# Optimization experiments

Measured on AMD Instinct MI355X. Metric: run time of the kernel, lower is better.

## Reference

```python
import jax, jax.numpy as jnp
import numpy as np

N, E, G, B, L = 24576, 98304, 512, 512, 1000
F_IN, H1, C1, C2, HID = 5, 2, 64, 128, 256


def setup_inputs() -> dict:
    key = jax.random.key(0)
    ks = jax.random.split(key, 20)
    rn = lambda k, s: jax.random.normal(k, s, jnp.float32) * 0.1
    return {
        "x": jax.random.normal(ks[0], (N, F_IN), jnp.float32),
        "edge_index": jax.random.randint(ks[1], (2, E), 0, N),
        "batch": jnp.sort(jax.random.randint(ks[2], (N,), 0, G)),
        "protein_seq": jax.random.randint(ks[3], (B, L), 0, 22),
        "W1": rn(ks[4], (F_IN, H1 * C1)), "att_src1": rn(ks[5], (H1, C1)), "att_dst1": rn(ks[6], (H1, C1)), "b1": jnp.zeros((H1 * C1,), jnp.float32),
        "W2": rn(ks[7], (H1 * C1, C2)), "att_src2": rn(ks[8], (1, C2)), "att_dst2": rn(ks[9], (1, C2)), "b2": jnp.zeros((C2,), jnp.float32),
        "Wd": rn(ks[10], (C2, HID)), "bd": jnp.zeros((HID,), jnp.float32),
        "Pe": rn(ks[11], (22, 64)),
        "K1": rn(ks[12], (64, 64, 3)), "bk1": jnp.zeros((64,), jnp.float32),
        "K2": rn(ks[13], (128, 64, 5)), "bk2": jnp.zeros((128,), jnp.float32),
        "Wp": rn(ks[14], (128, HID)), "bp": jnp.zeros((HID,), jnp.float32),
        "Wf1": rn(ks[15], (2 * HID, 128)), "bf1": jnp.zeros((128,), jnp.float32),
        "Wf2": rn(ks[16], (128, 64)), "bf2": jnp.zeros((64,), jnp.float32),
        "Wo": rn(ks[17], (64, 1)), "bo": jnp.zeros((1,), jnp.float32),
    }


def _gat(x, edge_index, W, att_src, att_dst, b, heads, out_ch):
    """PyG GATConv: add self-loops, per-edge LeakyReLU(0.2) scores, segment softmax over dst."""
    n = x.shape[0]
    h = (x @ W).reshape(n, heads, out_ch)
    loop = jnp.arange(n)
    src = jnp.concatenate([edge_index[0], loop])
    dst = jnp.concatenate([edge_index[1], loop])
    a_s = jnp.sum(h * att_src[None], axis=-1)  # [n, H]
    a_d = jnp.sum(h * att_dst[None], axis=-1)
    e = jax.nn.leaky_relu(a_s[src] + a_d[dst], negative_slope=0.2)  # [E+n, H]
    m = jax.ops.segment_max(e, dst, num_segments=n)
    w = jnp.exp(e - m[dst])
    den = jax.ops.segment_sum(w, dst, num_segments=n)
    alpha = w / (den[dst] + 1e-16)
    out = jax.ops.segment_sum(h[src] * alpha[..., None], dst, num_segments=n)
    return out.reshape(n, heads * out_ch) + b


def _conv1d(x, k, pad):  # x: [B,C,L], k: [O,I,K]
    return jax.lax.conv_general_dilated(x, k, (1,), [(pad, pad)], dimension_numbers=("NCH", "OIH", "NCH"))


def reference(x, edge_index, batch, protein_seq, W1, att_src1, att_dst1, b1, W2, att_src2, att_dst2, b2, Wd, bd, Pe, K1, bk1, K2, bk2, Wp, bp, Wf1, bf1, Wf2, bf2, Wo, bo):
    # drug branch (GAT x2 + global mean pool)
    g = jax.nn.elu(_gat(x, edge_index, W1, att_src1, att_dst1, b1, H1, C1))
    g = jax.nn.elu(_gat(g, edge_index, W2, att_src2, att_dst2, b2, 1, C2))
    sums = jax.ops.segment_sum(g, batch, num_segments=G)
    cnt = jax.ops.segment_sum(jnp.ones((g.shape[0], 1), g.dtype), batch, num_segments=G)
    drug = jax.nn.relu(sums / jnp.maximum(cnt, 1.0) @ Wd + bd)
    # protein branch (embed -> conv1d x2 -> global max pool)
    pe = Pe[protein_seq].transpose(0, 2, 1)  # [B, 64, L]
    p = jax.nn.elu(_conv1d(pe, K1, 1) + bk1[None, :, None])
    p = jax.nn.elu(_conv1d(p, K2, 2) + bk2[None, :, None])
    prot = jax.nn.relu(jnp.max(p, axis=2) @ Wp + bp)
    # head
    h = jnp.concatenate([drug, prot], axis=1)
    h = jax.nn.relu(h @ Wf1 + bf1)
    h = jax.nn.relu(h @ Wf2 + bf2)
    return h @ Wo + bo
```

## Files before the change

### kernel.cpp

```cpp
#include <hip/hip_runtime.h>
#include <hip/hip_bf16.h>
#include <math.h>

#define NN 24576
#define NE 98304
#define ETOT (NE + NN)
#define NG 512
#define NB 512
#define LL 1000
#define TL 124
#define NTILE 9
#define PROT_BLKS (NB * NTILE)
#define CNT_BLKS (ETOT / 256)
#define AS1_BLKS (NN * 2 / 256)

typedef __attribute__((ext_vector_type(8))) short short8;
typedef __attribute__((ext_vector_type(4))) short short4v;
typedef __attribute__((ext_vector_type(4))) float f32x4;

__device__ inline short f2bf(float x) {
    union { __hip_bfloat16 b; short s; } u;
    u.b = __float2bfloat16(x);
    return u.s;
}

__device__ inline float bf2f(short s) {
    return __uint_as_float(((unsigned)(unsigned short)s) << 16);
}

__device__ inline void atomicMaxFloat(float* addr, float val) {
    int* ai = (int*)addr;
    int old = __float_as_int(*addr);
    while (__int_as_float(old) < val) {
        int assumed = old;
        old = atomicCAS(ai, assumed, __float_as_int(val));
        if (old == assumed) break;
    }
}

__global__ void k_init_prep(int* deg, int* cursor, float* sums, float* cnt, float* pmax,
                            const float* K1, const float* K2, const float* W2, const float* Pe,
                            const float* W1, const float* as1c, const float* ad1c,
                            const float* as2c, const float* ad2c,
                            short* Bswz1, short* Bswz2, short* Bh2, short* Bl2, short* Peb,
                            float* wvec) {
    int bid = blockIdx.x, t = threadIdx.x;
    if (bid < 256) {
        int i = bid * 256 + t;
        if (i < NN) { deg[i] = 0; cursor[i] = 0; }
        if (i < NG * 128) sums[i] = 0.f;
        if (i < NG) cnt[i] = 0.f;
        if (i < NB * 128) pmax[i] = -1e30f;
        return;
    }
    int idx = (bid - 256) * 256 + t;
    if (idx < 22 * 64) Peb[idx] = f2bf(Pe[idx]);
    if (idx < 20) {
        int q = idx % 10, hd = q / 5, f = q % 5;
        const float* av = (idx < 10) ? as1c : ad1c;
        float s = 0.f;
        for (int c = 0; c < 64; c++) s += W1[f * 128 + hd * 64 + c] * av[hd * 64 + c];
        wvec[idx < 10 ? q : 10 + q] = s;
    }
    if (idx >= 32 && idx < 288) {
        int q = idx - 32;
        int kk = q & 127;
        const float* av = (q < 128) ? as2c : ad2c;
        float s = 0.f;
        for (int n2 = 0; n2 < 128; n2++) s += W2[kk * 128 + n2] * av[n2];
        wvec[idx] = s;
    }
    if (idx < 192 * 64) {
        int j = idx & 7, lane = (idx >> 3) & 63, rest = idx >> 9;
        int nt = rest & 3, kb = rest >> 2;
        int k = kb * 32 + ((lane >> 4) << 3) + j;
        int n = nt * 16 + (lane & 15);
        int kk = k >> 6, i = k & 63;
        Bswz1[idx] = f2bf(K1[n * 192 + i * 3 + kk]);
    }
    if (idx < 320 * 128) {
        int j = idx & 7, lane = (idx >> 3) & 63, rest = idx >> 9;
        int nt = rest & 7, kb = rest >> 3;
        int k = kb * 32 + ((lane >> 4) << 3) + j;
        int n = nt * 16 + (lane & 15);
        int kk = k / 64, i = k % 64;
        Bswz2[idx] = f2bf(K2[n * 320 + i * 5 + kk]);
    }
    if (idx < 128 * 128) {
        int j = idx & 7, lane = (idx >> 3) & 63, rest = idx >> 9;
        int nt = rest & 7, kb = rest >> 3;
        int k = kb * 32 + ((lane >> 4) << 3) + j;
        int n = nt * 16 + (lane & 15);
        float v = W2[k * 128 + n];
        short hh = f2bf(v);
        Bh2[idx] = hh;
        Bl2[idx] = f2bf(v - bf2f(hh));
    }
}

#define SSTR 72
__global__ __launch_bounds__(256, 4) void k_prot_cnt_as1(
    const int* seq, const short* Peb, const short* Bswz1, const float* bk1,
    const short* Bswz2, const float* bk2, float* pmax,
    const int* ei, int* deg,
    const float* x, const float* wvec, float* as1o, float* ad1o) {
    int bid = blockIdx.x;
    int t = threadIdx.x;

    if (bid >= PROT_BLKS) {
        int rb = bid - PROT_BLKS;
        if (rb < CNT_BLKS) {
            int e = rb * 256 + t;
            int d = (e < NE) ? ei[NE + e] : e - NE;
            atomicAdd(&deg[d], 1);
        } else {
            int idx = (rb - CNT_BLKS) * 256 + t;
            int n = idx >> 1, hd = idx & 1;
            float s = 0.f, dv = 0.f;
#pragma unroll
            for (int f = 0; f < 5; f++) {
                float xv = x[n * 5 + f];
                s += xv * wvec[hd * 5 + f];
                dv += xv * wvec[10 + hd * 5 + f];
            }
            as1o[idx] = s;
            ad1o[idx] = dv;
        }
        return;
    }

    __shared__ __align__(16) short sEmb[130 * SSTR];
    __shared__ __align__(16) short s1[132 * SSTR];

    int b = bid / NTILE;
    int tile = bid - b * NTILE;
    int t0 = tile * TL;
    int wv = t >> 6, lane = t & 63;
    int ln15 = lane & 15, quad = lane >> 4;
    int mhalf = wv & 1, nhalf = wv >> 1;

    for (int j0 = 0; j0 < 130; j0 += 64) {
        int j = j0 + (t >> 2);
        if (j < 130) {
            int c0 = (t & 3) * 16;
            int l = t0 - 3 + j;
            int id = (l >= 0 && l < LL) ? seq[b * LL + l] : -1;
            short* dst = &sEmb[j * SSTR + c0];
            if (id >= 0) {
                const short8* src = (const short8*)&Peb[id * 64 + c0];
                *(short8*)dst = src[0];
                *(short8*)(dst + 8) = src[1];
            } else {
                *(short8*)dst = (short8){0, 0, 0, 0, 0, 0, 0, 0};
                *(short8*)(dst + 8) = (short8){0, 0, 0, 0, 0, 0, 0, 0};
            }
        }
    }
    s1[(128 + (t >> 6)) * SSTR + (t & 63)] = 0;
    __syncthreads();

    {
        f32x4 acc[4][2];
#pragma unroll
        for (int mi = 0; mi < 4; mi++)
#pragma unroll
            for (int ni = 0; ni < 2; ni++) acc[mi][ni] = (f32x4){0.f, 0.f, 0.f, 0.f};
#pragma unroll
        for (int kb = 0; kb < 6; kb++) {
            int koff = kb * 32 + quad * 8;
            int kk = koff >> 6, i0 = koff & 63;
            short8 b0 = *(const short8*)&Bswz1[((kb * 4 + nhalf * 2 + 0) * 64 + lane) * 8];
            short8 b1 = *(const short8*)&Bswz1[((kb * 4 + nhalf * 2 + 1) * 64 + lane) * 8];
#pragma unroll
            for (int mi = 0; mi < 4; mi++) {
                int arow = (mhalf * 4 + mi) * 16 + ln15 + kk;
                short8 a = *(const short8*)&sEmb[arow * SSTR + i0];
                acc[mi][0] = __builtin_amdgcn_mfma_f32_16x16x32_bf16(a, b0, acc[mi][0], 0, 0, 0);
                acc[mi][1] = __builtin_amdgcn_mfma_f32_16x16x32_bf16(a, b1, acc[mi][1], 0, 0, 0);
            }
        }
#pragma unroll
        for (int mi = 0; mi < 4; mi++) {
            int mt = mhalf * 4 + mi;
#pragma unroll
            for (int ni = 0; ni < 2; ni++) {
                int col = (nhalf * 2 + ni) * 16 + ln15;
                float bias = bk1[col];
#pragma unroll
                for (int r = 0; r < 4; r++) {
                    int q = mt * 16 + quad * 4 + r;
                    int l = t0 - 2 + q;
                    float v = acc[mi][ni][r] + bias;
                    v = v > 0.f ? v : __expf(v) - 1.f;
                    s1[q * SSTR + col] = (l >= 0 && l < LL) ? f2bf(v) : (short)0;
                }
            }
        }
    }
    __syncthreads();

    f32x4 acc2[4][4];
#pragma unroll
    for (int mi = 0; mi < 4; mi++)
#pragma unroll
        for (int ni = 0; ni < 4; ni++) acc2[mi][ni] = (f32x4){0.f, 0.f, 0.f, 0.f};
#pragma unroll 2
    for (int kb = 0; kb < 10; kb++) {
        int koff = kb * 32 + quad * 8;
        int kk = koff >> 6, i0 = koff & 63;
        short8 a[4], bb[4];
#pragma unroll
        for (int mi = 0; mi < 4; mi++) {
            int arow = (mhalf * 4 + mi) * 16 + ln15 + kk;
            a[mi] = *(const short8*)&s1[arow * SSTR + i0];
        }
#pragma unroll
        for (int ni = 0; ni < 4; ni++)
            bb[ni] = *(const short8*)&Bswz2[((kb * 8 + nhalf * 4 + ni) * 64 + lane) * 8];
#pragma unroll
        for (int mi = 0; mi < 4; mi++)
#pragma unroll
            for (int ni = 0; ni < 4; ni++)
                acc2[mi][ni] = __builtin_amdgcn_mfma_f32_16x16x32_bf16(a[mi], bb[ni], acc2[mi][ni], 0, 0, 0);
    }

#pragma unroll
    for (int ni = 0; ni < 4; ni++) {
        int col = (nhalf * 4 + ni) * 16 + ln15;
        float mx = -1e30f;
#pragma unroll
        for (int mi = 0; mi < 4; mi++) {
#pragma unroll
            for (int r = 0; r < 4; r++) {
                int p = (mhalf * 4 + mi) * 16 + quad * 4 + r;
                if (p < TL && t0 + p < LL) mx = fmaxf(mx, acc2[mi][ni][r]);
            }
        }
        mx = fmaxf(mx, __shfl_xor(mx, 16, 64));
        mx = fmaxf(mx, __shfl_xor(mx, 32, 64));
        if (quad == 0) {
            float v = mx + bk2[col];
            v = v > 0.f ? v : __expf(v) - 1.f;
            atomicMaxFloat(&pmax[b * 128 + col], v);
        }
    }
}

__global__ void k_scan1(const int* deg, int* excl, int* part) {
    __shared__ int s[256];
    int b = blockIdx.x, t = threadIdx.x, i = b * 256 + t;
    int v = deg[i];
    s[t] = v;
    __syncthreads();
    for (int o = 1; o < 256; o <<= 1) {
        int x = (t >= o) ? s[t - o] : 0;
        __syncthreads();
        s[t] += x;
        __syncthreads();
    }
    excl[i] = s[t] - v;
    if (t == 255) part[b] = s[t];
}

__global__ void k_scan23(const int* excl, const int* part, int* rowptr) {
    __shared__ int sp[96];
    __shared__ int pref;
    int b = blockIdx.x, t = threadIdx.x;
    if (t < 96) sp[t] = part[t];
    __syncthreads();
    if (t == 0) {
        int run = 0;
        for (int i = 0; i < b; i++) run += sp[i];
        pref = run;
    }
    __syncthreads();
    int i = b * 256 + t;
    rowptr[i] = excl[i] + pref;
    if (i == 0) rowptr[NN] = ETOT;
}

__global__ void k_scatter(const int* ei, const int* rowptr, int* cursor, int* colidx) {
    int e = blockIdx.x * 256 + threadIdx.x;
    if (e >= ETOT) return;
    int s, d;
    if (e < NE) { s = ei[e]; d = ei[NE + e]; }
    else { s = d = e - NE; }
    int pos = atomicAdd(&cursor[d], 1);
    colidx[rowptr[d] + pos] = s;
}

__global__ void k_agg2x(const int* rowptr, const int* colidx, const float* x,
                        const float* as_, const float* ad_,
                        const float* W1, const float* b1, const float* wvec,
                        unsigned int* g1b, float* as2, float* ad2) {
    __shared__ float sW[640];
    __shared__ float sb1[128];
    __shared__ float swa[256];
    int t = threadIdx.x;
    for (int i = t; i < 640; i += 256) sW[i] = W1[i];
    if (t < 128) { sb1[t] = b1[t]; swa[t] = wvec[32 + t]; swa[128 + t] = wvec[160 + t]; }
    __syncthreads();

    int d = blockIdx.x * 16 + (t >> 4);
    int g = t & 15;
    int hd = (g < 5) ? 0 : 1;
    int f = (g < 5) ? g : g - 5;
    float adv = ad_[d * 2 + hd];
    int p0 = rowptr[d], p1 = rowptr[d + 1];
    float m = -1e30f, den = 0.f, acc = 0.f;
    if (g < 10) {
        for (int pc = p0; pc < p1; pc += 4) {
            int sarr[4]; float ev[4], xv[4];
#pragma unroll
            for (int i = 0; i < 4; i++) {
                int pp = pc + i;
                sarr[i] = colidx[pp < p1 ? pp : p1 - 1];
            }
#pragma unroll
            for (int i = 0; i < 4; i++) {
                ev[i] = as_[sarr[i] * 2 + hd];
                xv[i] = x[sarr[i] * 5 + f];
            }
#pragma unroll
            for (int i = 0; i < 4; i++) {
                if (pc + i < p1) {
                    float e = ev[i] + adv;
                    e = e >= 0.f ? e : 0.2f * e;
                    float nm = fmaxf(m, e);
                    float sc = __expf(m - nm);
                    float w = __expf(e - nm);
                    den = den * sc + w;
                    acc = acc * sc + w * xv[i];
                    m = nm;
                }
            }
        }
    }
    float xn = acc / (den + 1e-16f);
    int gb = (t & 63) & ~15;
    int hcol = g >> 3;
    float xs[5];
#pragma unroll
    for (int f2 = 0; f2 < 5; f2++)
        xs[f2] = __shfl(xn, gb + hcol * 5 + f2, 64);
    float ps = 0.f, pd = 0.f;
    float g1v[8];
#pragma unroll
    for (int k = 0; k < 8; k++) {
        int col = g * 8 + k;
        float v = sb1[col];
#pragma unroll
        for (int f2 = 0; f2 < 5; f2++) v += xs[f2] * sW[f2 * 128 + col];
        v = v > 0.f ? v : __expf(v) - 1.f;
        g1v[k] = v;
        ps += v * swa[col];
        pd += v * swa[128 + col];
    }
    uint4 pk;
    pk.x = ((unsigned)(unsigned short)f2bf(g1v[1]) << 16) | (unsigned)(unsigned short)f2bf(g1v[0]);
    pk.y = ((unsigned)(unsigned short)f2bf(g1v[3]) << 16) | (unsigned)(unsigned short)f2bf(g1v[2]);
    pk.z = ((unsigned)(unsigned short)f2bf(g1v[5]) << 16) | (unsigned)(unsigned short)f2bf(g1v[4]);
    pk.w = ((unsigned)(unsigned short)f2bf(g1v[7]) << 16) | (unsigned)(unsigned short)f2bf(g1v[6]);
    *(uint4*)&g1b[d * 64 + g * 4] = pk;
#pragma unroll
    for (int msk = 1; msk < 16; msk <<= 1) {
        ps += __shfl_xor(ps, msk, 64);
        pd += __shfl_xor(pd, msk, 64);
    }
    if (g == 0) { as2[d] = ps; ad2[d] = pd; }
}

__global__ void k_agg1y(const int* rowptr, const int* colidx, const unsigned int* hb,
                        const float* as_, const float* ad_, float* yacc) {
    int t = threadIdx.x;
    int d = blockIdx.x * 4 + (t >> 6);
    int c = t & 63;
    float adv = ad_[d];
    int p0 = rowptr[d], p1 = rowptr[d + 1];
    float m = -1e30f, den = 0.f, acc0 = 0.f, acc1 = 0.f;
    for (int pc = p0; pc < p1; pc += 4) {
        int sarr[4]; float ev[4]; unsigned int hv[4];
#pragma unroll
        for (int i = 0; i < 4; i++) {
            int pp = pc + i;
            sarr[i] = colidx[pp < p1 ? pp : p1 - 1];
        }
#pragma unroll
        for (int i = 0; i < 4; i++) {
            ev[i] = as_[sarr[i]];
            hv[i] = hb[sarr[i] * 64 + c];
        }
#pragma unroll
        for (int i = 0; i < 4; i++) {
            if (pc + i < p1) {
                float e = ev[i] + adv;
                e = e >= 0.f ? e : 0.2f * e;
                float nm = fmaxf(m, e);
                float sc = __expf(m - nm);
                float w = __expf(e - nm);
                den = den * sc + w;
                float h0 = __uint_as_float(hv[i] << 16);
                float h1v = __uint_as_float(hv[i] & 0xFFFF0000u);
                acc0 = acc0 * sc + w * h0;
                acc1 = acc1 * sc + w * h1v;
                m = nm;
            }
        }
    }
    float inv = 1.f / (den + 1e-16f);
    ((float2*)yacc)[d * 64 + c] = (float2){acc0 * inv, acc1 * inv};
}

#define ASTR 136
__global__ __launch_bounds__(256, 2) void k_g2mm(
    const float* yacc, const short* Bh, const short* Bl, const float* b2, float* g2) {
    __shared__ __align__(16) short Ah[64 * ASTR];
    __shared__ __align__(16) short Al[64 * ASTR];
    int t = threadIdx.x;
    int m0 = blockIdx.x * 64;
    int wv = t >> 6, lane = t & 63;
    int ln15 = lane & 15, quad = lane >> 4;

    for (int i = t; i < 64 * 32; i += 256) {
        int row = i >> 5, c4 = (i & 31) * 4;
        float4 v = *(const float4*)&yacc[(m0 + row) * 128 + c4];
        short4v hi, lo;
        hi.x = f2bf(v.x); lo.x = f2bf(v.x - bf2f(hi.x));
        hi.y = f2bf(v.y); lo.y = f2bf(v.y - bf2f(hi.y));
        hi.z = f2bf(v.z); lo.z = f2bf(v.z - bf2f(hi.z));
        hi.w = f2bf(v.w); lo.w = f2bf(v.w - bf2f(hi.w));
        *(short4v*)&Ah[row * ASTR + c4] = hi;
        *(short4v*)&Al[row * ASTR + c4] = lo;
    }
    __syncthreads();

    f32x4 acc[8];
#pragma unroll
    for (int nt = 0; nt < 8; nt++) acc[nt] = (f32x4){0.f, 0.f, 0.f, 0.f};
    int arow = wv * 16 + ln15;
#pragma unroll
    for (int kb = 0; kb < 4; kb++) {
        int koff = kb * 32 + quad * 8;
        short8 a_hi = *(const short8*)&Ah[arow * ASTR + koff];
        short8 a_lo = *(const short8*)&Al[arow * ASTR + koff];
#pragma unroll
        for (int nt = 0; nt < 8; nt++) {
            short8 bh = *(const short8*)&Bh[((kb * 8 + nt) * 64 + lane) * 8];
            short8 bl = *(const short8*)&Bl[((kb * 8 + nt) * 64 + lane) * 8];
            acc[nt] = __builtin_amdgcn_mfma_f32_16x16x32_bf16(a_hi, bh, acc[nt], 0, 0, 0);
            acc[nt] = __builtin_amdgcn_mfma_f32_16x16x32_bf16(a_hi, bl, acc[nt], 0, 0, 0);
            acc[nt] = __builtin_amdgcn_mfma_f32_16x16x32_bf16(a_lo, bh, acc[nt], 0, 0, 0);
        }
    }
#pragma unroll
    for (int nt = 0; nt < 8; nt++) {
        int col = nt * 16 + ln15;
        float bias = b2[col];
#pragma unroll
        for (int r = 0; r < 4; r++) {
            float v = acc[nt][r] + bias;
            v = v > 0.f ? v : __expf(v) - 1.f;
            int n = m0 + wv * 16 + quad * 4 + r;
            g2[n * 128 + col] = v;
        }
    }
}

__global__ void k_pool(const float* g2, const int* batch, float* sums, float* cnt) {
    __shared__ int sb[96];
    int blk = blockIdx.x, j = threadIdx.x;
    int n0 = blk * 96;
    if (j < 96) sb[j] = batch[n0 + j];
    __syncthreads();
    float v[4];
#pragma unroll
    for (int i = 0; i < 4; i++) v[i] = g2[(n0 + i) * 128 + j];
    int cur = sb[0], runStart = 0;
    float acc = 0.f;
    for (int q0 = 0; q0 < 96; q0 += 4) {
        float nv[4] = {0.f, 0.f, 0.f, 0.f};
        if (q0 + 4 < 96) {
#pragma unroll
            for (int i = 0; i < 4; i++) nv[i] = g2[(n0 + q0 + 4 + i) * 128 + j];
        }
#pragma unroll
        for (int i = 0; i < 4; i++) {
            int q = q0 + i;
            int bb = sb[q];
            if (bb != cur) {
                atomicAdd(&sums[cur * 128 + j], acc);
                if (j == 0) atomicAdd(&cnt[cur], (float)(q - runStart));
                cur = bb; acc = 0.f; runStart = q;
            }
            acc += v[i];
        }
#pragma unroll
        for (int i = 0; i < 4; i++) v[i] = nv[i];
    }
    atomicAdd(&sums[cur * 128 + j], acc);
    if (j == 0) atomicAdd(&cnt[cur], (float)(96 - runStart));
}

__global__ void k_tail(const float* pmax, const float* Wp, const float* bp,
                       const float* sums, const float* cnt, const float* Wd, const float* bd,
                       const float* Wf1, const float* bf1, const float* Wf2, const float* bf2,
                       const float* Wo, const float* bo, float* out) {
    __shared__ float in2[512];
    __shared__ float hh[128];
    __shared__ float h2s[64];
    int g = blockIdx.x, t = threadIdx.x;

    float pacc = bp[t];
#pragma unroll 8
    for (int i = 0; i < 128; i++) pacc += pmax[g * 128 + i] * Wp[i * 256 + t];
    in2[256 + t] = pacc > 0.f ? pacc : 0.f;

    float c = cnt[g]; c = c < 1.f ? 1.f : c;
    float inv = 1.f / c;
    float dacc = bd[t];
#pragma unroll 8
    for (int i = 0; i < 128; i++) dacc += sums[g * 128 + i] * inv * Wd[i * 256 + t];
    in2[t] = dacc > 0.f ? dacc : 0.f;
    __syncthreads();

    if (t < 128) {
        float acc = bf1[t];
#pragma unroll 8
        for (int cc = 0; cc < 512; cc++) acc += in2[cc] * Wf1[cc * 128 + t];
        hh[t] = acc > 0.f ? acc : 0.f;
    }
    __syncthreads();
    if (t < 64) {
        float a2 = bf2[t];
#pragma unroll 8
        for (int cc = 0; cc < 128; cc++) a2 += hh[cc] * Wf2[cc * 64 + t];
        h2s[t] = a2 > 0.f ? a2 : 0.f;
    }
    __syncthreads();
    if (t == 0) {
        float o = bo[0];
#pragma unroll 8
        for (int cc = 0; cc < 64; cc++) o += h2s[cc] * Wo[cc];
        out[g] = o;
    }
}

extern "C" void kernel_launch(void* const* d_in, const int* in_sizes, int n_in,
                              void* d_out, int out_size, void* d_ws, size_t ws_size,
                              hipStream_t stream) {
    (void)in_sizes; (void)n_in; (void)out_size; (void)ws_size;
    const float* x   = (const float*)d_in[0];
    const int* ei    = (const int*)d_in[1];
    const int* batch = (const int*)d_in[2];
    const int* seq   = (const int*)d_in[3];
    const float* W1  = (const float*)d_in[4];
    const float* a_s1 = (const float*)d_in[5];
    const float* a_d1 = (const float*)d_in[6];
    const float* b1  = (const float*)d_in[7];
    const float* W2  = (const float*)d_in[8];
    const float* a_s2 = (const float*)d_in[9];
    const float* a_d2 = (const float*)d_in[10];
    const float* b2  = (const float*)d_in[11];
    const float* Wd  = (const float*)d_in[12];
    const float* bd  = (const float*)d_in[13];
    const float* Pe  = (const float*)d_in[14];
    const float* K1  = (const float*)d_in[15];
    const float* bk1 = (const float*)d_in[16];
    const float* K2  = (const float*)d_in[17];
    const float* bk2 = (const float*)d_in[18];
    const float* Wp  = (const float*)d_in[19];
    const float* bp  = (const float*)d_in[20];
    const float* Wf1 = (const float*)d_in[21];
    const float* bf1 = (const float*)d_in[22];
    const float* Wf2 = (const float*)d_in[23];
    const float* bf2 = (const float*)d_in[24];
    const float* Wo  = (const float*)d_in[25];
    const float* bo  = (const float*)d_in[26];
    float* out = (float*)d_out;

    float* w = (float*)d_ws;
    float* g1bf = w; w += NN * 64;
    float* yacc = w; w += NN * 128;
    float* g2   = w; w += NN * 128;
    float* as1  = w; w += NN * 2;
    float* ad1  = w; w += NN * 2;
    float* as2  = w; w += NN;
    float* ad2  = w; w += NN;
    float* sums = w; w += NG * 128;
    float* cnt  = w; w += NG;
    float* pmax = w; w += NB * 128;
    float* wvec = w; w += 512;
    short* Bswz1 = (short*)w; w += 192 * 64 / 2;
    short* Bswz2 = (short*)w; w += 320 * 128 / 2;
    short* Bh2  = (short*)w; w += 128 * 128 / 2;
    short* Bl2  = (short*)w; w += 128 * 128 / 2;
    short* Peb  = (short*)w; w += 22 * 64 / 2 + 8;
    int* deg    = (int*)w; w += NN;
    int* cursor = (int*)w; w += NN;
    int* excl   = (int*)w; w += NN;
    int* part   = (int*)w; w += 128;
    int* rowptr = (int*)w; w += NN + 8;
    int* colidx = (int*)w; w += ETOT;

    unsigned int* g1b = (unsigned int*)g1bf;

    hipLaunchKernelGGL(k_init_prep, dim3(256 + 160), dim3(256), 0, stream,
                       deg, cursor, sums, cnt, pmax,
                       K1, K2, W2, Pe, W1, a_s1, a_d1, a_s2, a_d2,
                       Bswz1, Bswz2, Bh2, Bl2, Peb, wvec);

    hipLaunchKernelGGL(k_prot_cnt_as1, dim3(PROT_BLKS + CNT_BLKS + AS1_BLKS), dim3(256), 0, stream,
                       seq, Peb, Bswz1, bk1, Bswz2, bk2, pmax,
                       ei, deg, x, wvec, as1, ad1);

    hipLaunchKernelGGL(k_scan1, dim3(NN / 256), dim3(256), 0, stream, deg, excl, part);
    hipLaunchKernelGGL(k_scan23, dim3(NN / 256), dim3(256), 0, stream, excl, part, rowptr);
    hipLaunchKernelGGL(k_scatter, dim3(ETOT / 256), dim3(256), 0, stream, ei, rowptr, cursor, colidx);

    hipLaunchKernelGGL(k_agg2x, dim3(NN / 16), dim3(256), 0, stream,
                       rowptr, colidx, x, as1, ad1, W1, b1, wvec, g1b, as2, ad2);

    hipLaunchKernelGGL(k_agg1y, dim3(NN / 4), dim3(256), 0, stream,
                       rowptr, colidx, g1b, as2, ad2, yacc);

    hipLaunchKernelGGL(k_g2mm, dim3(NN / 64), dim3(256), 0, stream,
                       yacc, Bh2, Bl2, b2, g2);

    hipLaunchKernelGGL(k_pool, dim3(NN / 96), dim3(128), 0, stream, g2, batch, sums, cnt);

    hipLaunchKernelGGL(k_tail, dim3(NG), dim3(256), 0, stream,
                       pmax, Wp, bp, sums, cnt, Wd, bd, Wf1, bf1, Wf2, bf2, Wo, bo, out);
}
```

Baseline: 305.5 us.

## Fuse layer-2 aggregation, matmul and pooling; merge scans; drop softmax max

Fuses the second GAT aggregation, the bf16-split MFMA matmul and mean-pool accumulation into one kernel. The intermediate yacc and g2 buffers are no longer written to or read from global memory. The two-pass scan becomes a single kernel where each block recomputes its prefix from deg, and node counting moves into the earlier fused kernel. The online softmax max-subtraction is dropped in both aggregations, which removes exp work but risks overflow if attention scores get large. The fused kernel runs 16 sequential node aggregations per wave, which lowers parallelism for the gather phase.

```diff
diff --git a/kernel.cpp b/kernel.cpp
--- a/kernel.cpp
+++ b/kernel.cpp
@@ -13,6 +13,7 @@
 #define PROT_BLKS (NB * NTILE)
 #define CNT_BLKS (ETOT / 256)
 #define AS1_BLKS (NN * 2 / 256)
+#define BCNT_BLKS (NN / 256)
 
 typedef __attribute__((ext_vector_type(8))) short short8;
 typedef __attribute__((ext_vector_type(4))) short short4v;
@@ -103,7 +104,8 @@
     const int* seq, const short* Peb, const short* Bswz1, const float* bk1,
     const short* Bswz2, const float* bk2, float* pmax,
     const int* ei, int* deg,
-    const float* x, const float* wvec, float* as1o, float* ad1o) {
+    const float* x, const float* wvec, float* as1o, float* ad1o,
+    const int* batch, float* cnt) {
     int bid = blockIdx.x;
     int t = threadIdx.x;
 
@@ -113,7 +115,7 @@
             int e = rb * 256 + t;
             int d = (e < NE) ? ei[NE + e] : e - NE;
             atomicAdd(&deg[d], 1);
-        } else {
+        } else if (rb < CNT_BLKS + AS1_BLKS) {
             int idx = (rb - CNT_BLKS) * 256 + t;
             int n = idx >> 1, hd = idx & 1;
             float s = 0.f, dv = 0.f;
@@ -125,6 +127,9 @@
             }
             as1o[idx] = s;
             ad1o[idx] = dv;
+        } else {
+            int n = (rb - CNT_BLKS - AS1_BLKS) * 256 + t;
+            atomicAdd(&cnt[batch[n]], 1.f);
         }
         return;
     }
@@ -246,36 +251,27 @@
     }
 }
 
-__global__ void k_scan1(const int* deg, int* excl, int* part) {
+__global__ void k_rowptr(const int* deg, int* rowptr) {
     __shared__ int s[256];
+    __shared__ int red[4];
     int b = blockIdx.x, t = threadIdx.x, i = b * 256 + t;
     int v = deg[i];
     s[t] = v;
     __syncthreads();
     for (int o = 1; o < 256; o <<= 1) {
-        int x = (t >= o) ? s[t - o] : 0;
+        int xx = (t >= o) ? s[t - o] : 0;
         __syncthreads();
-        s[t] += x;
+        s[t] += xx;
         __syncthreads();
     }
-    excl[i] = s[t] - v;
-    if (t == 255) part[b] = s[t];
-}
-
-__global__ void k_scan23(const int* excl, const int* part, int* rowptr) {
-    __shared__ int sp[96];
-    __shared__ int pref;
-    int b = blockIdx.x, t = threadIdx.x;
-    if (t < 96) sp[t] = part[t];
-    __syncthreads();
-    if (t == 0) {
-        int run = 0;
-        for (int i = 0; i < b; i++) run += sp[i];
-        pref = run;
-    }
-    __syncthreads();
-    int i = b * 256 + t;
-    rowptr[i] = excl[i] + pref;
+    int excl = s[t] - v;
+    int psum = 0;
+    for (int k = t; k < b * 256; k += 256) psum += deg[k];
+    for (int off = 32; off > 0; off >>= 1) psum += __shfl_down(psum, off, 64);
+    if ((t & 63) == 0) red[t >> 6] = psum;
+    __syncthreads();
+    int pref = red[0] + red[1] + red[2] + red[3];
+    rowptr[i] = excl + pref;
     if (i == 0) rowptr[NN] = ETOT;
 }
 
@@ -307,7 +303,7 @@
     int f = (g < 5) ? g : g - 5;
     float adv = ad_[d * 2 + hd];
     int p0 = rowptr[d], p1 = rowptr[d + 1];
-    float m = -1e30f, den = 0.f, acc = 0.f;
+    float den = 0.f, acc = 0.f;
     if (g < 10) {
         for (int pc = p0; pc < p1; pc += 4) {
             int sarr[4]; float ev[4], xv[4];
@@ -326,12 +322,9 @@
                 if (pc + i < p1) {
                     float e = ev[i] + adv;
                     e = e >= 0.f ? e : 0.2f * e;
-                    float nm = fmaxf(m, e);
-                    float sc = __expf(m - nm);
-                    float w = __expf(e - nm);
-                    den = den * sc + w;
-                    acc = acc * sc + w * xv[i];
-                    m = nm;
+                    float w = __expf(e);
+                    den += w;
+                    acc += w * xv[i];
                 }
             }
         }
@@ -370,50 +363,11 @@
     if (g == 0) { as2[d] = ps; ad2[d] = pd; }
 }
 
-__global__ void k_agg1y(const int* rowptr, const int* colidx, const unsigned int* hb,
-                        const float* as_, const float* ad_, float* yacc) {
-    int t = threadIdx.x;
-    int d = blockIdx.x * 4 + (t >> 6);
-    int c = t & 63;
-    float adv = ad_[d];
-    int p0 = rowptr[d], p1 = rowptr[d + 1];
-    float m = -1e30f, den = 0.f, acc0 = 0.f, acc1 = 0.f;
-    for (int pc = p0; pc < p1; pc += 4) {
-        int sarr[4]; float ev[4]; unsigned int hv[4];
-#pragma unroll
-        for (int i = 0; i < 4; i++) {
-            int pp = pc + i;
-            sarr[i] = colidx[pp < p1 ? pp : p1 - 1];
-        }
-#pragma unroll
-        for (int i = 0; i < 4; i++) {
-            ev[i] = as_[sarr[i]];
-            hv[i] = hb[sarr[i] * 64 + c];
-        }
-#pragma unroll
-        for (int i = 0; i < 4; i++) {
-            if (pc + i < p1) {
-                float e = ev[i] + adv;
-                e = e >= 0.f ? e : 0.2f * e;
-                float nm = fmaxf(m, e);
-                float sc = __expf(m - nm);
-                float w = __expf(e - nm);
-                den = den * sc + w;
-                float h0 = __uint_as_float(hv[i] << 16);
-                float h1v = __uint_as_float(hv[i] & 0xFFFF0000u);
-                acc0 = acc0 * sc + w * h0;
-                acc1 = acc1 * sc + w * h1v;
-                m = nm;
-            }
-        }
-    }
-    float inv = 1.f / (den + 1e-16f);
-    ((float2*)yacc)[d * 64 + c] = (float2){acc0 * inv, acc1 * inv};
-}
-
 #define ASTR 136
-__global__ __launch_bounds__(256, 2) void k_g2mm(
-    const float* yacc, const short* Bh, const short* Bl, const float* b2, float* g2) {
+__global__ __launch_bounds__(256, 2) void k_aggmm(
+    const int* rowptr, const int* colidx, const unsigned int* hb,
+    const float* as_, const float* ad_, const short* Bh, const short* Bl,
+    const float* b2, const int* batch, float* sums) {
     __shared__ __align__(16) short Ah[64 * ASTR];
     __shared__ __align__(16) short Al[64 * ASTR];
     int t = threadIdx.x;
@@ -421,16 +375,44 @@
     int wv = t >> 6, lane = t & 63;
     int ln15 = lane & 15, quad = lane >> 4;
 
-    for (int i = t; i < 64 * 32; i += 256) {
-        int row = i >> 5, c4 = (i & 31) * 4;
-        float4 v = *(const float4*)&yacc[(m0 + row) * 128 + c4];
-        short4v hi, lo;
-        hi.x = f2bf(v.x); lo.x = f2bf(v.x - bf2f(hi.x));
-        hi.y = f2bf(v.y); lo.y = f2bf(v.y - bf2f(hi.y));
-        hi.z = f2bf(v.z); lo.z = f2bf(v.z - bf2f(hi.z));
-        hi.w = f2bf(v.w); lo.w = f2bf(v.w - bf2f(hi.w));
-        *(short4v*)&Ah[row * ASTR + c4] = hi;
-        *(short4v*)&Al[row * ASTR + c4] = lo;
+    for (int i = 0; i < 16; i++) {
+        int row = wv * 16 + i;
+        int d = m0 + row;
+        float adv = ad_[d];
+        int p0 = rowptr[d], p1 = rowptr[d + 1];
+        float den = 0.f, a0 = 0.f, a1 = 0.f;
+        for (int pc = p0; pc < p1; pc += 4) {
+            int sarr[4]; float ev[4]; unsigned int hv[4];
+#pragma unroll
+            for (int j = 0; j < 4; j++) {
+                int pp = pc + j;
+                sarr[j] = colidx[pp < p1 ? pp : p1 - 1];
+            }
+#pragma unroll
+            for (int j = 0; j < 4; j++) {
+                ev[j] = as_[sarr[j]];
+                hv[j] = hb[sarr[j] * 64 + lane];
+            }
+#pragma unroll
+            for (int j = 0; j < 4; j++) {
+                if (pc + j < p1) {
+                    float e = ev[j] + adv;
+                    e = e >= 0.f ? e : 0.2f * e;
+                    float w = __expf(e);
+                    den += w;
+                    a0 += w * __uint_as_float(hv[j] << 16);
+                    a1 += w * __uint_as_float(hv[j] & 0xFFFF0000u);
+                }
+            }
+        }
+        float inv = 1.f / (den + 1e-16f);
+        float v0 = a0 * inv, v1 = a1 * inv;
+        short h0 = f2bf(v0), h1 = f2bf(v1);
+        short l0 = f2bf(v0 - bf2f(h0)), l1 = f2bf(v1 - bf2f(h1));
+        *(unsigned int*)&Ah[row * ASTR + 2 * lane] =
+            ((unsigned)(unsigned short)h1 << 16) | (unsigned)(unsigned short)h0;
+        *(unsigned int*)&Al[row * ASTR + 2 * lane] =
+            ((unsigned)(unsigned short)l1 << 16) | (unsigned)(unsigned short)l0;
     }
     __syncthreads();
 
@@ -452,53 +434,34 @@
             acc[nt] = __builtin_amdgcn_mfma_f32_16x16x32_bf16(a_lo, bh, acc[nt], 0, 0, 0);
         }
     }
+
+    int nbase = m0 + wv * 16 + quad * 4;
+    int bg[4];
+#pragma unroll
+    for (int r = 0; r < 4; r++) bg[r] = batch[nbase + r];
 #pragma unroll
     for (int nt = 0; nt < 8; nt++) {
         int col = nt * 16 + ln15;
         float bias = b2[col];
+        float vv[4];
 #pragma unroll
         for (int r = 0; r < 4; r++) {
             float v = acc[nt][r] + bias;
-            v = v > 0.f ? v : __expf(v) - 1.f;
-            int n = m0 + wv * 16 + quad * 4 + r;
-            g2[n * 128 + col] = v;
-        }
-    }
-}
-
-__global__ void k_pool(const float* g2, const int* batch, float* sums, float* cnt) {
-    __shared__ int sb[96];
-    int blk = blockIdx.x, j = threadIdx.x;
-    int n0 = blk * 96;
-    if (j < 96) sb[j] = batch[n0 + j];
-    __syncthreads();
-    float v[4];
-#pragma unroll
-    for (int i = 0; i < 4; i++) v[i] = g2[(n0 + i) * 128 + j];
-    int cur = sb[0], runStart = 0;
-    float acc = 0.f;
-    for (int q0 = 0; q0 < 96; q0 += 4) {
-        float nv[4] = {0.f, 0.f, 0.f, 0.f};
-        if (q0 + 4 < 96) {
-#pragma unroll
-            for (int i = 0; i < 4; i++) nv[i] = g2[(n0 + q0 + 4 + i) * 128 + j];
-        }
-#pragma unroll
-        for (int i = 0; i < 4; i++) {
-            int q = q0 + i;
-            int bb = sb[q];
-            if (bb != cur) {
-                atomicAdd(&sums[cur * 128 + j], acc);
-                if (j == 0) atomicAdd(&cnt[cur], (float)(q - runStart));
-                cur = bb; acc = 0.f; runStart = q;
-            }
-            acc += v[i];
-        }
-#pragma unroll
-        for (int i = 0; i < 4; i++) v[i] = nv[i];
-    }
-    atomicAdd(&sums[cur * 128 + j], acc);
-    if (j == 0) atomicAdd(&cnt[cur], (float)(96 - runStart));
+            vv[r] = v > 0.f ? v : __expf(v) - 1.f;
+        }
+        int cur = bg[0];
+        float a = vv[0];
+#pragma unroll
+        for (int r = 1; r < 4; r++) {
+            if (bg[r] == cur) a += vv[r];
+            else {
+                atomicAdd(&sums[cur * 128 + col], a);
+                cur = bg[r];
+                a = vv[r];
+            }
+        }
+        atomicAdd(&sums[cur * 128 + col], a);
+    }
 }
 
 __global__ void k_tail(const float* pmax, const float* Wp, const float* bp,
@@ -580,8 +543,6 @@
 
     float* w = (float*)d_ws;
     float* g1bf = w; w += NN * 64;
-    float* yacc = w; w += NN * 128;
-    float* g2   = w; w += NN * 128;
     float* as1  = w; w += NN * 2;
     float* ad1  = w; w += NN * 2;
     float* as2  = w; w += NN;
@@ -597,8 +558,6 @@
     short* Peb  = (short*)w; w += 22 * 64 / 2 + 8;
     int* deg    = (int*)w; w += NN;
     int* cursor = (int*)w; w += NN;
-    int* excl   = (int*)w; w += NN;
-    int* part   = (int*)w; w += 128;
     int* rowptr = (int*)w; w += NN + 8;
     int* colidx = (int*)w; w += ETOT;
 
@@ -609,24 +568,20 @@
                        K1, K2, W2, Pe, W1, a_s1, a_d1, a_s2, a_d2,
                        Bswz1, Bswz2, Bh2, Bl2, Peb, wvec);
 
-    hipLaunchKernelGGL(k_prot_cnt_as1, dim3(PROT_BLKS + CNT_BLKS + AS1_BLKS), dim3(256), 0, stream,
+    hipLaunchKernelGGL(k_prot_cnt_as1,
+                       dim3(PROT_BLKS + CNT_BLKS + AS1_BLKS + BCNT_BLKS), dim3(256), 0, stream,
                        seq, Peb, Bswz1, bk1, Bswz2, bk2, pmax,
-                       ei, deg, x, wvec, as1, ad1);
-
-    hipLaunchKernelGGL(k_scan1, dim3(NN / 256), dim3(256), 0, stream, deg, excl, part);
-    hipLaunchKernelGGL(k_scan23, dim3(NN / 256), dim3(256), 0, stream, excl, part, rowptr);
+                       ei, deg, x, wvec, as1, ad1, batch, cnt);
+
+    hipLaunchKernelGGL(k_rowptr, dim3(NN / 256), dim3(256), 0, stream, deg, rowptr);
+
     hipLaunchKernelGGL(k_scatter, dim3(ETOT / 256), dim3(256), 0, stream, ei, rowptr, cursor, colidx);
 
     hipLaunchKernelGGL(k_agg2x, dim3(NN / 16), dim3(256), 0, stream,
                        rowptr, colidx, x, as1, ad1, W1, b1, wvec, g1b, as2, ad2);
 
-    hipLaunchKernelGGL(k_agg1y, dim3(NN / 4), dim3(256), 0, stream,
-                       rowptr, colidx, g1b, as2, ad2, yacc);
-
-    hipLaunchKernelGGL(k_g2mm, dim3(NN / 64), dim3(256), 0, stream,
-                       yacc, Bh2, Bl2, b2, g2);
-
-    hipLaunchKernelGGL(k_pool, dim3(NN / 96), dim3(128), 0, stream, g2, batch, sums, cnt);
+    hipLaunchKernelGGL(k_aggmm, dim3(NN / 64), dim3(256), 0, stream,
+                       rowptr, colidx, g1b, as2, ad2, Bh2, Bl2, b2, batch, sums);
 
     hipLaunchKernelGGL(k_tail, dim3(NG), dim3(256), 0, stream,
                        pmax, Wp, bp, sums, cnt, Wd, bd, Wf1, bf1, Wf2, bf2, Wo, bo, out);
```

Measured after the change: 340.2 us. 11.4% more time.
